# Kernel optimization log

Measured on AMD Instinct MI355X. Metric: run time of the kernel, lower is better.

Reference implementation:

```python
import jax, jax.numpy as jnp
import numpy as np

D_MODEL = 1024
NUM_HEADS = 16
HEAD_DIM = D_MODEL // NUM_HEADS


def setup_inputs() -> dict:
    key = jax.random.key(0)
    ks = jax.random.split(key, 5)
    B, S = 4, 2048
    x = jax.random.normal(ks[0], (B, S, D_MODEL), dtype=jnp.float32)
    scale = 1.0 / np.sqrt(D_MODEL)
    qkv_w = jax.random.normal(ks[1], (3 * D_MODEL, D_MODEL), dtype=jnp.float32) * scale
    qkv_b = jnp.zeros((3 * D_MODEL,), dtype=jnp.float32)
    out_w = jax.random.normal(ks[2], (D_MODEL, D_MODEL), dtype=jnp.float32) * scale
    out_b = jnp.zeros((D_MODEL,), dtype=jnp.float32)
    return {"x": x, "qkv_w": qkv_w, "qkv_b": qkv_b, "out_w": out_w, "out_b": out_b}


def reference(x, qkv_w, qkv_b, out_w, out_b):
    B, S, _ = x.shape
    # qkv projection (torch Linear: x @ W.T + b)
    qkv = x @ qkv_w.T + qkv_b  # [B, S, 3*D]
    q, k, v = jnp.split(qkv, 3, axis=-1)
    # [B, H, S, hd]
    q = q.reshape(B, S, NUM_HEADS, HEAD_DIM).transpose(0, 2, 1, 3)
    k = k.reshape(B, S, NUM_HEADS, HEAD_DIM).transpose(0, 2, 1, 3)
    v = v.reshape(B, S, NUM_HEADS, HEAD_DIM).transpose(0, 2, 1, 3)
    scores = jnp.einsum('bhqd,bhkd->bhqk', q, k) / np.sqrt(HEAD_DIM).astype(np.float32)
    attn = jax.nn.softmax(scores, axis=-1)
    context = jnp.einsum('bhqk,bhkd->bhqd', attn, v)  # [B, H, S, hd]
    context = context.transpose(0, 2, 1, 3).reshape(B, S, D_MODEL)
    return context @ out_w.T + out_b
```

## Files before the change

kernel.cpp:

```cpp
#include <hip/hip_runtime.h>
#include <hip/hip_bf16.h>
#include <math.h>

#define D_MODEL 1024
#define NHEADS  16
#define HDIM    64
#define BATCH   4
#define SLEN    2048
#define MROWS   (BATCH * SLEN)
#define QKV_N   (3 * D_MODEL)

typedef __attribute__((ext_vector_type(8))) short bhalf8;
typedef __attribute__((ext_vector_type(4))) float f32x4;

#if __has_builtin(__builtin_amdgcn_exp2f)
#define EXP2(x) __builtin_amdgcn_exp2f(x)
#else
#define EXP2(x) exp2f(x)
#endif

#define MFMA16(a, b, c) __builtin_amdgcn_mfma_f32_16x16x32_bf16((a), (b), (c), 0, 0, 0)

static __device__ __forceinline__ unsigned short f2bf(float f) {
    unsigned int u = __builtin_bit_cast(unsigned int, f);
    unsigned int r = (u + 0x7FFFu + ((u >> 16) & 1u)) >> 16;
    return (unsigned short)r;
}

static __device__ __forceinline__ unsigned int pack_hi16(float lo, float hi) {
    return __builtin_amdgcn_perm(__builtin_bit_cast(unsigned int, hi),
                                 __builtin_bit_cast(unsigned int, lo),
                                 0x07060302u);
}

static __device__ __forceinline__ void load_lds16(const void* g, void* l) {
    __builtin_amdgcn_global_load_lds(
        (const __attribute__((address_space(1))) void*)g,
        (__attribute__((address_space(3))) void*)l, 16, 0, 0);
}

#define FENCE() __asm__ volatile("" ::: "memory")
#define BARRIER() do { FENCE();                                   \
        __builtin_amdgcn_sched_barrier(0);                        \
        __builtin_amdgcn_s_barrier();                             \
        __builtin_amdgcn_sched_barrier(0); FENCE(); } while (0)
#define WAIT_VM(N)   __asm__ volatile("s_waitcnt vmcnt(" #N ")" ::: "memory")
#define WAIT_LGKM0() __asm__ volatile("s_waitcnt lgkmcnt(0)" ::: "memory")

__global__ __launch_bounds__(256) void cast3_f32_bf16(
    const float* __restrict__ a, unsigned short* __restrict__ oa, int na,
    const float* __restrict__ b, unsigned short* __restrict__ ob, int nb,
    const float* __restrict__ c, unsigned short* __restrict__ oc, int nc)
{
    int i = (blockIdx.x * 256 + threadIdx.x) * 4;
    const float* src;
    unsigned short* dst;
    if (i < na)           { src = a + i;            dst = oa + i; }
    else if (i < na + nb) { src = b + (i - na);     dst = ob + (i - na); }
    else {
        int j = i - na - nb;
        if (j >= nc) return;
        src = c + j; dst = oc + j;
    }
    float4 v = *(const float4*)src;
    ushort4 o;
    o.x = f2bf(v.x); o.y = f2bf(v.y); o.z = f2bf(v.z); o.w = f2bf(v.w);
    *(ushort4*)dst = o;
}

template<bool BF16OUT>
__global__ __launch_bounds__(256) void gemm_mfma_bt(
    const unsigned short* __restrict__ A,
    const unsigned short* __restrict__ W,
    const float* __restrict__ bias,
    void* __restrict__ outv,
    int M, int N, int K, int qcols, float qscale)
{
    __shared__ __align__(16) unsigned short As[128 * 32];
    __shared__ __align__(16) unsigned short Bs[128 * 32];

    int bxs = blockIdx.x, bys = blockIdx.y;
    {
        const int nx  = gridDim.x;
        const int nwg = nx * gridDim.y;
        if ((nwg & 7) == 0) {
            const int orig = bys * nx + bxs;
            const int nf   = (orig & 7) * (nwg >> 3) + (orig >> 3);
            bxs = nf % nx;
            bys = nf / nx;
        }
    }

    const int tid  = threadIdx.x;
    const int bm   = bys * 128;
    const int bn   = bxs * 128;
    const int wave = tid >> 6;
    const int lane = tid & 63;
    const int m16  = lane & 15;
    const int quad = lane >> 4;
    const int wm   = (wave & 1) * 64;
    const int wn   = (wave >> 1) * 64;

    const int r0 = tid >> 2;
    const int s0 = tid & 3;
    const int g0 = (s0 - (r0 >> 1)) & 3;
    const int g1 = (s0 - ((r0 + 64) >> 1)) & 3;

    const size_t arow0 = (size_t)(bm + r0) * K + g0 * 8;
    const size_t arow1 = (size_t)(bm + r0 + 64) * K + g1 * 8;
    const size_t brow0 = (size_t)(bn + r0) * K + g0 * 8;
    const size_t brow1 = (size_t)(bn + r0 + 64) * K + g1 * 8;

    f32x4 acc[4][4];
    f32x4 zero = {0.f, 0.f, 0.f, 0.f};
#pragma unroll
    for (int i = 0; i < 4; ++i)
#pragma unroll
        for (int j = 0; j < 4; ++j) acc[i][j] = zero;

    for (int kt = 0; kt < K; kt += 32) {
        __syncthreads();
        load_lds16(A + arow0 + kt, As + tid * 8);
        load_lds16(A + arow1 + kt, As + 2048 + tid * 8);
        load_lds16(W + brow0 + kt, Bs + tid * 8);
        load_lds16(W + brow1 + kt, Bs + 2048 + tid * 8);
        __asm__ volatile("s_waitcnt vmcnt(0)" ::: "memory");
        __syncthreads();

        bhalf8 af[4], bf[4];
#pragma unroll
        for (int i = 0; i < 4; ++i) {
            int ra = wm + i * 16 + m16;
            int sa = (quad + (ra >> 1)) & 3;
            af[i] = *(const bhalf8*)&As[ra * 32 + sa * 8];
        }
#pragma unroll
        for (int j = 0; j < 4; ++j) {
            int rb = wn + j * 16 + m16;
            int sb = (quad + (rb >> 1)) & 3;
            bf[j] = *(const bhalf8*)&Bs[rb * 32 + sb * 8];
        }
#pragma unroll
        for (int i = 0; i < 4; ++i)
#pragma unroll
            for (int j = 0; j < 4; ++j)
                acc[i][j] = __builtin_amdgcn_mfma_f32_16x16x32_bf16(
                    af[i], bf[j], acc[i][j], 0, 0, 0);
    }

    float bj[4], scj[4];
#pragma unroll
    for (int j = 0; j < 4; ++j) {
        int col = bn + wn + j * 16 + m16;
        bj[j]  = bias[col];
        scj[j] = (col < qcols) ? qscale : 1.0f;
    }

#pragma unroll
    for (int i = 0; i < 4; ++i) {
#pragma unroll
        for (int r = 0; r < 4; ++r) {
            size_t row = (size_t)(bm + wm + i * 16 + quad * 4 + r);
            if (BF16OUT) {
                unsigned short* dst = (unsigned short*)outv + row * N + bn + wn;
#pragma unroll
                for (int j = 0; j < 4; ++j)
                    dst[j * 16 + m16] = f2bf((acc[i][j][r] + bj[j]) * scj[j]);
            } else {
                float* dst = (float*)outv + row * N + bn + wn;
#pragma unroll
                for (int j = 0; j < 4; ++j)
                    dst[j * 16 + m16] = (acc[i][j][r] + bj[j]) * scj[j];
            }
        }
    }
}

__global__ __launch_bounds__(256, 4) void attn_mfma_kernel(
    const unsigned short* __restrict__ qkv, unsigned short* __restrict__ ctx)
{
    const int orig = blockIdx.x + (blockIdx.y << 4) + (blockIdx.z << 8);
    const int flat = ((orig & 7) << 7) | (orig >> 3);
    const int qt = flat & 15;
    const int h  = (flat >> 4) & 15;
    const int b  = flat >> 8;

    const int tid  = threadIdx.x;
    const int wave = tid >> 6;
    const int lane = tid & 63;
    const int m16  = lane & 15;
    const int quad = lane >> 4;

    __shared__ __align__(16) unsigned short K_lds[64 * 64];
    __shared__ __align__(16) unsigned short Vt_lds[64 * 72];
    __shared__ __align__(16) unsigned short QP_lds[4 * 32 * 72];

    const int srow  = tid >> 3;
    const int sslot = tid & 7;
    const int gk    = (sslot - srow) & 7;

    const int u    = tid & 31;
    const int k0   = (u & 15) | ((u & 16) << 1);
    const int idx0 = (u & 15) * 4 + ((u >> 4) << 1);
    const int vd0  = (tid >> 5) * 8;

    const unsigned short* kPtr =
        qkv + ((size_t)b * SLEN) * QKV_N + D_MODEL + h * HDIM
            + (size_t)srow * QKV_N + gk * 8;
    const unsigned short* vPtr0 =
        qkv + ((size_t)b * SLEN) * QKV_N + 2 * D_MODEL + h * HDIM
            + (size_t)k0 * QKV_N + vd0;
    const unsigned short* vPtr1 = vPtr0 + (size_t)16 * QKV_N;

    uint4 va_A, vb_A, va_B, vb_B;

#define ISSUE_K(T) do {                                                      \
        const unsigned short* kb_ = kPtr + (size_t)(T) * 64 * QKV_N;         \
        load_lds16(kb_,                        K_lds + tid * 8);             \
        load_lds16(kb_ + (size_t)32 * QKV_N,   K_lds + 2048 + tid * 8);      \
    } while (0)

#define ISSUE_V(T, VA, VB) do {                                              \
        VA = *(const uint4*)(vPtr0 + (size_t)(T) * 64 * QKV_N);              \
        VB = *(const uint4*)(vPtr1 + (size_t)(T) * 64 * QKV_N);              \
    } while (0)

#define WRITE_V(VA, VB) do {                                                                         \
        *(unsigned int*)&Vt_lds[(vd0 + 0) * 72 + idx0] = __builtin_amdgcn_perm(VB.x, VA.x, 0x05040100u); \
        *(unsigned int*)&Vt_lds[(vd0 + 1) * 72 + idx0] = __builtin_amdgcn_perm(VB.x, VA.x, 0x07060302u); \
        *(unsigned int*)&Vt_lds[(vd0 + 2) * 72 + idx0] = __builtin_amdgcn_perm(VB.y, VA.y, 0x05040100u); \
        *(unsigned int*)&Vt_lds[(vd0 + 3) * 72 + idx0] = __builtin_amdgcn_perm(VB.y, VA.y, 0x07060302u); \
        *(unsigned int*)&Vt_lds[(vd0 + 4) * 72 + idx0] = __builtin_amdgcn_perm(VB.z, VA.z, 0x05040100u); \
        *(unsigned int*)&Vt_lds[(vd0 + 5) * 72 + idx0] = __builtin_amdgcn_perm(VB.z, VA.z, 0x07060302u); \
        *(unsigned int*)&Vt_lds[(vd0 + 6) * 72 + idx0] = __builtin_amdgcn_perm(VB.w, VA.w, 0x05040100u); \
        *(unsigned int*)&Vt_lds[(vd0 + 7) * 72 + idx0] = __builtin_amdgcn_perm(VB.w, VA.w, 0x07060302u); \
    } while (0)

    {
        const unsigned short* qbase =
            qkv + (size_t)(b * SLEN + qt * 128) * QKV_N + h * HDIM;
#pragma unroll
        for (int c = 0; c < 4; ++c) {
            int r = c * 32 + srow;
            int g = (sslot - r) & 7;
            load_lds16(qbase + (size_t)r * QKV_N + g * 8,
                       QP_lds + c * 2048 + tid * 8);
        }
    }
    ISSUE_K(0);
    ISSUE_V(0, va_A, vb_A);
    WAIT_VM(2);
    BARRIER();

    bhalf8 qf[2][2];
#pragma unroll
    for (int qi = 0; qi < 2; ++qi) {
        int rq = wave * 32 + qi * 16 + m16;
#pragma unroll
        for (int ks = 0; ks < 2; ++ks) {
            int slot = (ks * 4 + quad + rq) & 7;
            qf[qi][ks] = *(const bhalf8*)&QP_lds[rq * 64 + slot * 8];
        }
    }

    WAIT_VM(0);
    WRITE_V(va_A, vb_A);
    ISSUE_V(1, va_B, vb_B);
    WAIT_LGKM0();
    BARRIER();

    f32x4 zero = {0.f, 0.f, 0.f, 0.f};
    f32x4 oacc[2][4], oacc_l[2];
#pragma unroll
    for (int qi = 0; qi < 2; ++qi) {
        oacc_l[qi] = zero;
#pragma unroll
        for (int dt = 0; dt < 4; ++dt) oacc[qi][dt] = zero;
    }

    bhalf8 ones;
#pragma unroll
    for (int i = 0; i < 8; ++i) ones[i] = (short)0x3F80;

    unsigned short* P = &QP_lds[wave * (32 * 72)];
    f32x4 sacc[2][4];

#define QKT_PHASE() do {                                                     \
        _Pragma("unroll")                                                    \
        for (int qi = 0; qi < 2; ++qi)                                       \
            _Pragma("unroll")                                                \
            for (int nt = 0; nt < 4; ++nt) sacc[qi][nt] = zero;              \
        __builtin_amdgcn_s_setprio(1);                                       \
        _Pragma("unroll")                                                    \
        for (int ks = 0; ks < 2; ++ks) {                                     \
            _Pragma("unroll")                                                \
            for (int nt = 0; nt < 4; ++nt) {                                 \
                int rk = nt * 16 + m16;                                      \
                int slot = (ks * 4 + quad + rk) & 7;                         \
                bhalf8 kf = *(const bhalf8*)&K_lds[rk * 64 + slot * 8];      \
                sacc[0][nt] = MFMA16(qf[0][ks], kf, sacc[0][nt]);            \
                sacc[1][nt] = MFMA16(qf[1][ks], kf, sacc[1][nt]);            \
            }                                                                \
        }                                                                    \
        __builtin_amdgcn_s_setprio(0);                                       \
    } while (0)

#define SOFTMAX_PHASE() do {                                                 \
        _Pragma("unroll")                                                    \
        for (int qi = 0; qi < 2; ++qi) {                                     \
            _Pragma("unroll")                                                \
            for (int r = 0; r < 4; ++r) {                                    \
                float p0 = EXP2(sacc[qi][0][r]);                             \
                float p1 = EXP2(sacc[qi][1][r]);                             \
                float p2 = EXP2(sacc[qi][2][r]);                             \
                float p3 = EXP2(sacc[qi][3][r]);                             \
                uint2 w;                                                     \
                w.x = pack_hi16(p0, p1);                                     \
                w.y = pack_hi16(p2, p3);                                     \
                *(uint2*)&P[(qi * 16 + quad * 4 + r) * 72 + m16 * 4] = w;    \
            }                                                                \
        }                                                                    \
        WAIT_LGKM0();                                                        \
        __builtin_amdgcn_sched_barrier(0);                                   \
    } while (0)

#define PV_PHASE() do {                                                      \
        __builtin_amdgcn_s_setprio(1);                                       \
        _Pragma("unroll")                                                    \
        for (int ks = 0; ks < 2; ++ks) {                                     \
            bhalf8 pf0 = *(const bhalf8*)&P[(m16)      * 72 + ks * 32 + quad * 8]; \
            bhalf8 pf1 = *(const bhalf8*)&P[(16 + m16) * 72 + ks * 32 + quad * 8]; \
            oacc_l[0] = MFMA16(pf0, ones, oacc_l[0]);                        \
            oacc_l[1] = MFMA16(pf1, ones, oacc_l[1]);                        \
            _Pragma("unroll")                                                \
            for (int dt = 0; dt < 4; ++dt) {                                 \
                bhalf8 vf = *(const bhalf8*)&Vt_lds[(dt * 16 + m16) * 72 + ks * 32 + quad * 8]; \
                oacc[0][dt] = MFMA16(pf0, vf, oacc[0][dt]);                  \
                oacc[1][dt] = MFMA16(pf1, vf, oacc[1][dt]);                  \
            }                                                                \
        }                                                                    \
        __builtin_amdgcn_s_setprio(0);                                       \
    } while (0)

#define TILE_FULL(T, VWA, VWB, VLA, VLB) do {                                \
        QKT_PHASE();                                                         \
        BARRIER();                     \
        ISSUE_K((T) + 1);                                                    \
        SOFTMAX_PHASE();                                                     \
        PV_PHASE();                                                          \
        BARRIER();                     \
        WAIT_VM(2);                     \
        WRITE_V(VWA, VWB);                                                   \
        ISSUE_V((T) + 2, VLA, VLB);                                          \
        WAIT_VM(2);                     \
        WAIT_LGKM0();                                                        \
        BARRIER();                           \
    } while (0)

    for (int t2 = 0; t2 < 30; t2 += 2) {
        TILE_FULL(t2,     va_B, vb_B, va_A, vb_A);
        TILE_FULL(t2 + 1, va_A, vb_A, va_B, vb_B);
    }

    QKT_PHASE();
    BARRIER();
    ISSUE_K(31);
    SOFTMAX_PHASE();
    PV_PHASE();
    BARRIER();
    WAIT_VM(2);
    WRITE_V(va_B, vb_B);
    WAIT_VM(0);
    WAIT_LGKM0();
    BARRIER();

    QKT_PHASE();
    SOFTMAX_PHASE();
    PV_PHASE();

#undef TILE_FULL
#undef PV_PHASE
#undef SOFTMAX_PHASE
#undef QKT_PHASE
#undef WRITE_V
#undef ISSUE_V
#undef ISSUE_K

#pragma unroll
    for (int qi = 0; qi < 2; ++qi) {
#pragma unroll
        for (int r = 0; r < 4; ++r) {
            float inv = 1.0f / oacc_l[qi][r];
            int row = b * SLEN + qt * 128 + wave * 32 + qi * 16 + quad * 4 + r;
            unsigned short* dst = ctx + (size_t)row * D_MODEL + h * HDIM;
#pragma unroll
            for (int dt = 0; dt < 4; ++dt)
                dst[dt * 16 + m16] = f2bf(oacc[qi][dt][r] * inv);
        }
    }
}

extern "C" void kernel_launch(void* const* d_in, const int* in_sizes, int n_in,
                              void* d_out, int out_size, void* d_ws, size_t ws_size,
                              hipStream_t stream)
{
    const float* x     = (const float*)d_in[0];
    const float* qkv_w = (const float*)d_in[1];
    const float* qkv_b = (const float*)d_in[2];
    const float* out_w = (const float*)d_in[3];
    const float* out_b = (const float*)d_in[4];
    float* out = (float*)d_out;

    unsigned short* xbf  = (unsigned short*)d_ws;
    unsigned short* wqkv = xbf  + (size_t)MROWS * D_MODEL;
    unsigned short* wout = wqkv + (size_t)QKV_N * D_MODEL;
    unsigned short* qkv  = wout + (size_t)D_MODEL * D_MODEL;
    unsigned short* ctx  = qkv  + (size_t)MROWS * QKV_N;

    {
        const int na = MROWS * D_MODEL;
        const int nb = QKV_N * D_MODEL;
        const int nc = D_MODEL * D_MODEL;
        const int total = na + nb + nc;
        cast3_f32_bf16<<<total / 1024, 256, 0, stream>>>(
            x, xbf, na, qkv_w, wqkv, nb, out_w, wout, nc);
    }

    const float QSCALE = 0.125f * 1.44269504088896f;

    {
        dim3 grid(QKV_N / 128, MROWS / 128);
        gemm_mfma_bt<true><<<grid, 256, 0, stream>>>(xbf, wqkv, qkv_b, qkv,
                                                     MROWS, QKV_N, D_MODEL,
                                                     D_MODEL, QSCALE);
    }

    {
        dim3 grid(SLEN / 128, NHEADS, BATCH);
        attn_mfma_kernel<<<grid, 256, 0, stream>>>(qkv, ctx);
    }

    {
        dim3 grid(D_MODEL / 128, MROWS / 128);
        gemm_mfma_bt<false><<<grid, 256, 0, stream>>>(ctx, wout, out_b, out,
                                                      MROWS, D_MODEL, D_MODEL,
                                                      0, 1.0f);
    }
}
```

Measured before the change: 273.2 us.

## Triple-buffer LDS tiles in projection GEMM to overlap loads with MFMA

Replaces the load-wait-compute loop in the bf16 projection GEMM with a three-slot LDS ring. The global-to-LDS copy for tile t+2 is issued before tile t is computed, and only the oldest loads are waited on, so memory latency overlaps with MFMA work and the loop needs one barrier per tile instead of two. It also raises wave priority around the MFMA block. In exchange, LDS use triples to 48KB per block, which may reduce occupancy. The unrolled loop assumes K/32 leaves a remainder of 2 when divided by 3, which holds for K=1024.

```diff
diff --git a/kernel.cpp b/kernel.cpp
--- a/kernel.cpp
+++ b/kernel.cpp
@@ -76,8 +76,8 @@
     void* __restrict__ outv,
     int M, int N, int K, int qcols, float qscale)
 {
-    __shared__ __align__(16) unsigned short As[128 * 32];
-    __shared__ __align__(16) unsigned short Bs[128 * 32];
+    __shared__ __align__(16) unsigned short As[3][128 * 32];
+    __shared__ __align__(16) unsigned short Bs[3][128 * 32];
 
     int bxs = blockIdx.x, bys = blockIdx.y;
     {
@@ -118,35 +118,56 @@
 #pragma unroll
         for (int j = 0; j < 4; ++j) acc[i][j] = zero;
 
-    for (int kt = 0; kt < K; kt += 32) {
-        __syncthreads();
-        load_lds16(A + arow0 + kt, As + tid * 8);
-        load_lds16(A + arow1 + kt, As + 2048 + tid * 8);
-        load_lds16(W + brow0 + kt, Bs + tid * 8);
-        load_lds16(W + brow1 + kt, Bs + 2048 + tid * 8);
-        __asm__ volatile("s_waitcnt vmcnt(0)" ::: "memory");
-        __syncthreads();
-
-        bhalf8 af[4], bf[4];
-#pragma unroll
-        for (int i = 0; i < 4; ++i) {
-            int ra = wm + i * 16 + m16;
-            int sa = (quad + (ra >> 1)) & 3;
-            af[i] = *(const bhalf8*)&As[ra * 32 + sa * 8];
-        }
-#pragma unroll
-        for (int j = 0; j < 4; ++j) {
-            int rb = wn + j * 16 + m16;
-            int sb = (quad + (rb >> 1)) & 3;
-            bf[j] = *(const bhalf8*)&Bs[rb * 32 + sb * 8];
-        }
-#pragma unroll
-        for (int i = 0; i < 4; ++i)
-#pragma unroll
-            for (int j = 0; j < 4; ++j)
-                acc[i][j] = __builtin_amdgcn_mfma_f32_16x16x32_bf16(
-                    af[i], bf[j], acc[i][j], 0, 0, 0);
-    }
+#define G_STAGE(T, SLOT) do {                                        \
+        const int ko_ = (T) << 5;                                    \
+        load_lds16(A + arow0 + ko_, As[SLOT] + tid * 8);             \
+        load_lds16(A + arow1 + ko_, As[SLOT] + 2048 + tid * 8);      \
+        load_lds16(W + brow0 + ko_, Bs[SLOT] + tid * 8);             \
+        load_lds16(W + brow1 + ko_, Bs[SLOT] + 2048 + tid * 8);      \
+    } while (0)
+
+#define G_COMPUTE(CUR) do {                                          \
+        bhalf8 af[4], bf[4];                                         \
+        _Pragma("unroll")                                            \
+        for (int i = 0; i < 4; ++i) {                                \
+            int ra = wm + i * 16 + m16;                              \
+            int sa = (quad + (ra >> 1)) & 3;                         \
+            af[i] = *(const bhalf8*)&As[CUR][ra * 32 + sa * 8];      \
+        }                                                            \
+        _Pragma("unroll")                                            \
+        for (int j = 0; j < 4; ++j) {                                \
+            int rb = wn + j * 16 + m16;                              \
+            int sb = (quad + (rb >> 1)) & 3;                         \
+            bf[j] = *(const bhalf8*)&Bs[CUR][rb * 32 + sb * 8];      \
+        }                                                            \
+        __builtin_amdgcn_s_setprio(1);                               \
+        _Pragma("unroll")                                            \
+        for (int i = 0; i < 4; ++i)                                  \
+            _Pragma("unroll")                                        \
+            for (int j = 0; j < 4; ++j)                              \
+                acc[i][j] = MFMA16(af[i], bf[j], acc[i][j]);         \
+        __builtin_amdgcn_s_setprio(0);                               \
+    } while (0)
+
+    G_STAGE(0, 0);
+    G_STAGE(1, 1);
+    WAIT_VM(4);
+    BARRIER();
+
+    const int NT = K >> 5;
+    for (int t3 = 0; t3 < NT - 2; t3 += 3) {
+        G_STAGE(t3 + 2, 2); G_COMPUTE(0); WAIT_VM(4); BARRIER();
+        G_STAGE(t3 + 3, 0); G_COMPUTE(1); WAIT_VM(4); BARRIER();
+        G_STAGE(t3 + 4, 1); G_COMPUTE(2); WAIT_VM(4); BARRIER();
+    }
+
+    G_COMPUTE(0);
+    WAIT_VM(0);
+    BARRIER();
+    G_COMPUTE(1);
+
+#undef G_COMPUTE
+#undef G_STAGE
 
     float bj[4], scj[4];
 #pragma unroll
```

Result: faster. 263.1 us (-3.7%).
